# Optimization experiments

Hardware: AMD Instinct MI355X
Metric: run time of the kernel (lower is better)

The kernel has to match this reference:

```python
import jax, jax.numpy as jnp
import numpy as np
from jax import lax

B, C1, C2, CM, H, W, K = 8, 256, 256, 128, 80, 80, 3
N = K * K
PAD = 1
EPS = 1e-5  # nn.BatchNorm2d default eps


def _bn(x, g, b, m, v):
    # eval-mode BatchNorm2d, NCHW
    inv = g / jnp.sqrt(v + EPS)
    return x * inv[None, :, None, None] + (b - m * inv)[None, :, None, None]


def _conv1x1(x, w):  # w: [O, I]
    return jnp.einsum('bihw,oi->bohw', x, w)


def _conv3x3(x, w, b):  # w: [O, I, 3, 3]
    y = lax.conv_general_dilated(x, w, window_strides=(1, 1),
                                 padding=((PAD, PAD), (PAD, PAD)),
                                 dimension_numbers=('NCHW', 'OIHW', 'NCHW'))
    return y + b[None, :, None, None]


def _deform_conv2d(x, offset, mask, w, bias):
    # DCNv2 (torchvision deform_conv2d semantics), stride=1, pad=1, k=3.
    # x: [B,C,H,W]; offset: [B,2N,H,W] pairs (dy,dx) per kernel tap (row-major);
    # mask: [B,N,H,W]; w: [O,C,3,3]
    Bx, C, Hx, Wx = x.shape
    ky, kx = jnp.meshgrid(jnp.arange(K), jnp.arange(K), indexing='ij')
    ky = ky.reshape(N).astype(x.dtype)
    kx = kx.reshape(N).astype(x.dtype)
    off = offset.reshape(Bx, N, 2, Hx, Wx)
    # sampling positions [B,N,H,W]
    py = (jnp.arange(Hx, dtype=x.dtype)[None, None, :, None] - PAD
          + ky[None, :, None, None] + off[:, :, 0])
    px = (jnp.arange(Wx, dtype=x.dtype)[None, None, None, :] - PAD
          + kx[None, :, None, None] + off[:, :, 1])

    y0 = jnp.floor(py)
    x0 = jnp.floor(px)
    wy1 = py - y0  # frac weights
    wx1 = px - x0
    x_flat = x.reshape(Bx, C, Hx * Wx)

    def corner(yi, xi, wgt):
        valid = (yi >= 0) & (yi < Hx) & (xi >= 0) & (xi < Wx)
        yc = jnp.clip(yi, 0, Hx - 1).astype(jnp.int32)
        xc = jnp.clip(xi, 0, Wx - 1).astype(jnp.int32)
        idx = (yc * Wx + xc).reshape(Bx, 1, N * Hx * Wx)
        g = jnp.take_along_axis(x_flat, idx, axis=2).reshape(Bx, C, N, Hx, Wx)
        return g * (wgt * valid.astype(x.dtype))[:, None]

    sampled = (corner(y0, x0, (1 - wy1) * (1 - wx1))
               + corner(y0, x0 + 1, (1 - wy1) * wx1)
               + corner(y0 + 1, x0, wy1 * (1 - wx1))
               + corner(y0 + 1, x0 + 1, wy1 * wx1))
    sampled = sampled * mask[:, None]  # modulated (v2)
    out = jnp.einsum('bcnhw,ocn->bohw', sampled, w.reshape(w.shape[0], C, N))
    return out + bias[None, :, None, None]


def setup_inputs() -> dict:
    key = jax.random.key(0)
    ks = jax.random.split(key, 20)
    f32 = jnp.float32
    d = {}
    d['x'] = jax.random.normal(ks[0], (B, C1, H, W), dtype=f32)
    # cv1: 1x1 conv (no bias) + BN
    d['cv1_w'] = jax.random.normal(ks[1], (CM, C1), dtype=f32) * (1.0 / np.sqrt(C1))
    d['bn1_g'] = jax.random.uniform(ks[2], (CM,), dtype=f32, minval=0.5, maxval=1.5)
    d['bn1_b'] = jax.random.normal(ks[3], (CM,), dtype=f32) * 0.1
    d['bn1_m'] = jax.random.normal(ks[4], (CM,), dtype=f32) * 0.1
    d['bn1_v'] = jax.random.uniform(ks[5], (CM,), dtype=f32, minval=0.5, maxval=1.5)
    # offset conv: predicts 3*N channels (2N offsets + N mask logits)
    d['off_w'] = jax.random.normal(ks[6], (3 * N, CM, K, K), dtype=f32) * 0.01
    d['off_b'] = jax.random.normal(ks[7], (3 * N,), dtype=f32) * 0.1
    # deformable conv main weight/bias
    d['dcn_w'] = jax.random.normal(ks[8], (CM, CM, K, K), dtype=f32) * np.sqrt(2.0 / (CM * N))
    d['dcn_b'] = jnp.zeros((CM,), dtype=f32)
    d['bn2_g'] = jax.random.uniform(ks[9], (CM,), dtype=f32, minval=0.5, maxval=1.5)
    d['bn2_b'] = jax.random.normal(ks[10], (CM,), dtype=f32) * 0.1
    d['bn2_m'] = jax.random.normal(ks[11], (CM,), dtype=f32) * 0.1
    d['bn2_v'] = jax.random.uniform(ks[12], (CM,), dtype=f32, minval=0.5, maxval=1.5)
    # cv3: 1x1 conv + BN
    d['cv3_w'] = jax.random.normal(ks[13], (C2, CM), dtype=f32) * (1.0 / np.sqrt(CM))
    d['bn3_g'] = jax.random.uniform(ks[14], (C2,), dtype=f32, minval=0.5, maxval=1.5)
    d['bn3_b'] = jax.random.normal(ks[15], (C2,), dtype=f32) * 0.1
    d['bn3_m'] = jax.random.normal(ks[16], (C2,), dtype=f32) * 0.1
    d['bn3_v'] = jax.random.uniform(ks[17], (C2,), dtype=f32, minval=0.5, maxval=1.5)
    return d


def reference(x, cv1_w, bn1_g, bn1_b, bn1_m, bn1_v,
              off_w, off_b, dcn_w, dcn_b,
              bn2_g, bn2_b, bn2_m, bn2_v,
              cv3_w, bn3_g, bn3_b, bn3_m, bn3_v):
    y = jax.nn.silu(_bn(_conv1x1(x, cv1_w), bn1_g, bn1_b, bn1_m, bn1_v))
    pred = _conv3x3(y, off_w, off_b)          # [B,3N,H,W]
    offset = pred[:, :2 * N]
    mask = jax.nn.sigmoid(pred[:, 2 * N:])
    y = _deform_conv2d(y, offset, mask, dcn_w, dcn_b)
    y = jax.nn.silu(_bn(y, bn2_g, bn2_b, bn2_m, bn2_v))
    y = jax.nn.silu(_bn(_conv1x1(y, cv3_w), bn3_g, bn3_b, bn3_m, bn3_v))
    return x + y  # shortcut: c1 == c2
```

## Files before the change

kernel.cpp:

```cpp
#include <hip/hip_runtime.h>
#include <math.h>

#define HWX   6400
#define WID   80
#define HGT   80
#define CMID  128
#define CIN   256
#define COUT  256

#define WS_PRED 0
#define WS_BN   1382400
#define WS_Y2   1383424
#define WS_Z2   4660224
#define WS_WPK  7937024
#define WS_WPO  8010752
#define WS_WP1  8029184
#define WS_WP3  8045568

typedef float floatx16 __attribute__((ext_vector_type(16)));
typedef short shortx8  __attribute__((ext_vector_type(8)));
typedef float floatx2  __attribute__((ext_vector_type(2)));

union U8 { uint32_t u[4]; shortx8 s; };

__device__ __forceinline__ float silu_f(float t){ return t / (1.f + __expf(-t)); }
__device__ __forceinline__ float bf16lo(uint32_t u){ return __uint_as_float(u << 16); }
__device__ __forceinline__ float bf16hi(uint32_t u){ return __uint_as_float(u & 0xffff0000u); }
__device__ __forceinline__ uint32_t f2bf(float f){
    uint32_t u = __float_as_uint(f);
    return (u + 0x7fffu + ((u >> 16) & 1u)) >> 16;
}
__device__ __forceinline__ floatx2 up2(uint32_t u){
    floatx2 r; r.x = __uint_as_float(u << 16); r.y = __uint_as_float(u & 0xffff0000u); return r;
}
__device__ __forceinline__ uint32_t pk2(floatx2 v){
    return __builtin_amdgcn_perm(__float_as_uint(v.y) + 0x8000u,
                                 __float_as_uint(v.x) + 0x8000u, 0x07060302u);
}
__device__ __forceinline__ uint32_t pk2f(float a, float b){ floatx2 v; v.x=a; v.y=b; return pk2(v); }

__global__ __launch_bounds__(256) void k0_prep(
    const float* __restrict__ dcn_w, const float* __restrict__ off_w,
    const float* __restrict__ cv1_w, const float* __restrict__ cv3_w,
    const float* __restrict__ g1, const float* __restrict__ b1, const float* __restrict__ m1, const float* __restrict__ v1,
    const float* __restrict__ g2, const float* __restrict__ b2, const float* __restrict__ m2, const float* __restrict__ v2,
    const float* __restrict__ dcn_b,
    const float* __restrict__ g3, const float* __restrict__ b3, const float* __restrict__ m3, const float* __restrict__ v3,
    uint32_t* __restrict__ wpk, uint32_t* __restrict__ wpo,
    uint32_t* __restrict__ wp1, uint32_t* __restrict__ wp3, float* __restrict__ bnw)
{
    int i = blockIdx.x * 256 + threadIdx.x;
    if (i < 4*9*8*256) {
        int j = i & 3, lane = (i >> 2) & 63, s = (i >> 8) & 7;
        int r2 = i >> 11; int tap = r2 % 9, g = r2 / 9;
        int oc = g*32 + (lane & 31);
        int c  = s*16 + ((lane >> 5) << 3) + 2*j;
        wpk[i] = f2bf(dcn_w[(oc*128 + c)*9 + tap]) | (f2bf(dcn_w[(oc*128 + c + 1)*9 + tap]) << 16);
    }
    if (i < 9*8*256) {
        int j = i & 3, lane = (i >> 2) & 63, s = (i >> 8) & 7, tap = i >> 11;
        int oc = lane & 31;
        int c  = s*16 + ((lane >> 5) << 3) + 2*j;
        float lo = (oc < 27) ? off_w[(oc*128 + c)*9 + tap] : 0.f;
        float hi = (oc < 27) ? off_w[(oc*128 + c + 1)*9 + tap] : 0.f;
        wpo[i] = f2bf(lo) | (f2bf(hi) << 16);
    }
    if (i < 4*16*256) {
        int j = i & 3, lane = (i >> 2) & 63, s = (i >> 8) & 15, g = i >> 12;
        int oc = g*32 + (lane & 31);
        int c  = s*16 + ((lane >> 5) << 3) + 2*j;
        wp1[i] = f2bf(cv1_w[oc*256 + c]) | (f2bf(cv1_w[oc*256 + c + 1]) << 16);
    }
    if (i < 8*8*256) {
        int j = i & 3, lane = (i >> 2) & 63, s = (i >> 8) & 7, g = i >> 11;
        int oc = g*32 + (lane & 31);
        int c  = s*16 + ((lane >> 5) << 3) + 2*j;
        wp3[i] = f2bf(cv3_w[oc*128 + c]) | (f2bf(cv3_w[oc*128 + c + 1]) << 16);
    }
    if (i < 128) {
        float inv = g1[i] * rsqrtf(v1[i] + 1e-5f);
        bnw[i] = inv; bnw[128+i] = b1[i] - m1[i]*inv;
    } else if (i < 256) {
        int j = i - 128;
        float inv = g2[j] * rsqrtf(v2[j] + 1e-5f);
        bnw[256+j] = inv; bnw[384+j] = b2[j] - m2[j]*inv + inv*dcn_b[j];
    } else if (i < 512) {
        int j = i - 256;
        float inv = g3[j] * rsqrtf(v3[j] + 1e-5f);
        bnw[512+j] = inv; bnw[768+j] = b3[j] - m3[j]*inv;
    }
}

#define K1PAD 68
__global__ __launch_bounds__(256) void k1_cv1(
    const float* __restrict__ x, const uint32_t* __restrict__ wp1,
    const float* __restrict__ bn, uint32_t* __restrict__ y2)
{
    __shared__ uint32_t L[64*66];
    int blk = blockIdx.x;
    int b = blk / 100, pix0 = (blk % 100) * 64;
    int t = threadIdx.x;
    int lane = t & 63, w = t >> 6;
    int pixl = lane & 31, bhalf = lane >> 5;
    floatx16 acc0 = {}, acc1 = {};
    const float* xb = x + (size_t)b*CIN*HWX + pix0;
    const uint32_t* wpg = wp1 + (size_t)(w*16)*256 + lane*4;

    int r2 = t >> 4, c4 = (t & 15) * 4;
    for (int kk = 0; kk < 256; kk += 32) {
        float4 a0 = *(const float4*)(xb + (size_t)(kk + 2*r2)*HWX + c4);
        float4 a1 = *(const float4*)(xb + (size_t)(kk + 2*r2 + 1)*HWX + c4);
        uint4 q;
        q.x = pk2f(a0.x, a1.x);
        q.y = pk2f(a0.y, a1.y);
        q.z = pk2f(a0.z, a1.z);
        q.w = pk2f(a0.w, a1.w);
        __syncthreads();
        *(uint4*)&L[r2*K1PAD + c4] = q;
        __syncthreads();
        #pragma unroll
        for (int sl = 0; sl < 2; sl++) {
            int s = (kk >> 4) + sl;
            U8 a, b0, b1;
            const uint32_t* as = wpg + s*256;
            a.u[0]=as[0]; a.u[1]=as[1]; a.u[2]=as[2]; a.u[3]=as[3];
            int row = sl*8 + bhalf*4;
            #pragma unroll
            for (int j = 0; j < 4; j++) b0.u[j] = L[(row+j)*K1PAD + pixl];
            #pragma unroll
            for (int j = 0; j < 4; j++) b1.u[j] = L[(row+j)*K1PAD + 32 + pixl];
            acc0 = __builtin_amdgcn_mfma_f32_32x32x16_bf16(a.s, b0.s, acc0, 0, 0, 0);
            acc1 = __builtin_amdgcn_mfma_f32_32x32x16_bf16(a.s, b1.s, acc1, 0, 0, 0);
        }
    }
    __syncthreads();
    #pragma unroll
    for (int r = 0; r < 16; r += 2) {
        int oc = w*32 + (r & 3) + 8*(r >> 2) + 4*bhalf;
        float s0 = bn[oc],   be0 = bn[128+oc];
        float s1 = bn[oc+1], be1 = bn[128+oc+1];
        uint32_t d0 = pk2f(silu_f(acc0[r]*s0+be0), silu_f(acc0[r+1]*s1+be1));
        uint32_t d1 = pk2f(silu_f(acc1[r]*s0+be0), silu_f(acc1[r+1]*s1+be1));
        int oc2 = oc >> 1;
        L[pixl*66 + oc2]        = d0;
        L[(32+pixl)*66 + oc2]   = d1;
    }
    __syncthreads();
    uint32_t* y2b = y2 + (size_t)b*HWX*64 + (size_t)pix0*64;
    int q2 = t & 31, p0 = t >> 5;
    #pragma unroll
    for (int pp = 0; pp < 8; pp++) {
        int pix = p0 + pp*8;
        uint2 v = make_uint2(L[pix*66 + q2*2], L[pix*66 + q2*2 + 1]);
        *(uint2*)(y2b + (size_t)pix*64 + q2*2) = v;
    }
}

__global__ __launch_bounds__(256) void k2_off(
    const uint32_t* __restrict__ y2, const uint32_t* __restrict__ wpo,
    const float* __restrict__ ob, float* __restrict__ pred)
{
    int blk = blockIdx.x;
    int b = blk / 50, pix0 = (blk % 50) * 128;
    int t = threadIdx.x;
    int lane = t & 63, w = t >> 6;
    int pixl = lane & 31, half = lane >> 5;
    int p = pix0 + w*32 + pixl;
    int h = p / WID, xw = p % WID;
    const uint32_t* yb = y2 + (size_t)b*HWX*64;
    floatx16 acc = {};

    for (int tap = 0; tap < 9; tap++) {
        int dy = tap/3 - 1, dx = tap%3 - 1;
        int gh = h + dy, gx = xw + dx;
        bool valid = (gh >= 0) && (gh < HGT) && (gx >= 0) && (gx < WID);
        const uint32_t* pp = yb + (size_t)(gh*WID + gx)*64 + half*4;
        const uint32_t* ap = wpo + (size_t)(tap*8)*256 + lane*4;
        #pragma unroll
        for (int s = 0; s < 8; s++) {
            U8 a, bf;
            const uint32_t* as = ap + s*256;
            a.u[0]=as[0]; a.u[1]=as[1]; a.u[2]=as[2]; a.u[3]=as[3];
            if (valid) {
                uint4 q = *(const uint4*)(pp + s*8);
                bf.u[0]=q.x; bf.u[1]=q.y; bf.u[2]=q.z; bf.u[3]=q.w;
            } else {
                bf.u[0]=0u; bf.u[1]=0u; bf.u[2]=0u; bf.u[3]=0u;
            }
            acc = __builtin_amdgcn_mfma_f32_32x32x16_bf16(a.s, bf.s, acc, 0, 0, 0);
        }
    }
    float* pb = pred + (size_t)b*27*HWX;
    #pragma unroll
    for (int r = 0; r < 16; r++) {
        int oc = (r & 3) + 8*(r >> 2) + 4*half;
        if (oc < 27) {
            float v = acc[r] + ob[oc];
            if (oc >= 18) v = 1.f/(1.f+__expf(-v));
            pb[oc*HWX + p] = v;
        }
    }
}

#define S2S 33
__global__ __launch_bounds__(256) void k3_dcn(
    const uint32_t* __restrict__ y2, const float* __restrict__ pred,
    const uint32_t* __restrict__ wpk, const float* __restrict__ bn, uint32_t* __restrict__ z2)
{
    __shared__ uint32_t S2[64*S2S];
    __shared__ int   sidx[32][4];
    __shared__ float swgt[32][4];
    int blk = blockIdx.x;
    int b = blk / 200, pix0 = (blk % 200) * 32;
    int t = threadIdx.x;
    int lane = t & 63, w = t >> 6;
    int pixl = lane & 31, bhalf = lane >> 5;
    const float* pb = pred + (size_t)b*27*HWX;
    const uint32_t* yb = y2 + (size_t)b*HWX*64;
    floatx16 acc = {};
    int c4 = lane & 31, pixoff = lane >> 5;

    for (int tap = 0; tap < 9; tap++) {
        __syncthreads();
        if (t < 32) {
            int pix = pix0 + t;
            int h = pix / WID, wq = pix % WID;
            float dy = pb[(2*tap)*HWX + pix];
            float dx = pb[(2*tap+1)*HWX + pix];
            float mk = pb[(18+tap)*HWX + pix];
            float pyf = (float)(h - 1 + tap/3) + dy;
            float pxf = (float)(wq - 1 + tap%3) + dx;
            float y0f = floorf(pyf), x0f = floorf(pxf);
            float wy1 = pyf - y0f, wx1 = pxf - x0f;
            int iy0 = (int)y0f, ix0 = (int)x0f;
            int iy1 = iy0 + 1,  ix1 = ix0 + 1;
            float vy0 = (iy0 >= 0 && iy0 < HGT) ? 1.f : 0.f;
            float vy1 = (iy1 >= 0 && iy1 < HGT) ? 1.f : 0.f;
            float vx0 = (ix0 >= 0 && ix0 < WID) ? 1.f : 0.f;
            float vx1 = (ix1 >= 0 && ix1 < WID) ? 1.f : 0.f;
            int cy0 = min(max(iy0,0),HGT-1), cy1 = min(max(iy1,0),HGT-1);
            int cx0 = min(max(ix0,0),WID-1), cx1 = min(max(ix1,0),WID-1);
            sidx[t][0] = cy0*WID+cx0; sidx[t][1] = cy0*WID+cx1;
            sidx[t][2] = cy1*WID+cx0; sidx[t][3] = cy1*WID+cx1;
            swgt[t][0] = (1.f-wy1)*(1.f-wx1)*mk*vy0*vx0;
            swgt[t][1] = (1.f-wy1)*wx1*mk*vy0*vx1;
            swgt[t][2] = wy1*(1.f-wx1)*mk*vy1*vx0;
            swgt[t][3] = wy1*wx1*mk*vy1*vx1;
        }
        __syncthreads();
        #pragma unroll
        for (int p = 0; p < 4; p++) {
            int pix = w*8 + p*2 + pixoff;
            int i0 = sidx[pix][0], i1 = sidx[pix][1], i2 = sidx[pix][2], i3 = sidx[pix][3];
            floatx2 W0, W1, W2, W3;
            W0.x = W0.y = swgt[pix][0]; W1.x = W1.y = swgt[pix][1];
            W2.x = W2.y = swgt[pix][2]; W3.x = W3.y = swgt[pix][3];
            uint2 u0 = *(const uint2*)(yb + (size_t)i0*64 + c4*2);
            uint2 u1 = *(const uint2*)(yb + (size_t)i1*64 + c4*2);
            uint2 u2 = *(const uint2*)(yb + (size_t)i2*64 + c4*2);
            uint2 u3 = *(const uint2*)(yb + (size_t)i3*64 + c4*2);
            floatx2 aX = up2(u0.x) * W0;
            aX = __builtin_elementwise_fma(up2(u1.x), W1, aX);
            aX = __builtin_elementwise_fma(up2(u2.x), W2, aX);
            aX = __builtin_elementwise_fma(up2(u3.x), W3, aX);
            floatx2 aY = up2(u0.y) * W0;
            aY = __builtin_elementwise_fma(up2(u1.y), W1, aY);
            aY = __builtin_elementwise_fma(up2(u2.y), W2, aY);
            aY = __builtin_elementwise_fma(up2(u3.y), W3, aY);
            S2[(c4*2)*S2S + pix]     = pk2(aX);
            S2[(c4*2 + 1)*S2S + pix] = pk2(aY);
        }
        __syncthreads();
        const uint32_t* wp = wpk + (size_t)((w*9 + tap)*8)*256 + lane*4;
        int kb = bhalf * 4;
        #pragma unroll
        for (int s = 0; s < 8; s++) {
            U8 a, bf;
            const uint32_t* wps = wp + s*256;
            a.u[0] = wps[0]; a.u[1] = wps[1]; a.u[2] = wps[2]; a.u[3] = wps[3];
            int c2b = s*8 + kb;
            bf.u[0] = S2[(c2b+0)*S2S + pixl];
            bf.u[1] = S2[(c2b+1)*S2S + pixl];
            bf.u[2] = S2[(c2b+2)*S2S + pixl];
            bf.u[3] = S2[(c2b+3)*S2S + pixl];
            acc = __builtin_amdgcn_mfma_f32_32x32x16_bf16(a.s, bf.s, acc, 0, 0, 0);
        }
    }
    __syncthreads();
    #pragma unroll
    for (int r = 0; r < 16; r += 2) {
        int oc = w*32 + (r & 3) + 8*(r >> 2) + 4*bhalf;
        float s0 = bn[256+oc],   be0 = bn[384+oc];
        float s1 = bn[256+oc+1], be1 = bn[384+oc+1];
        uint32_t d = pk2f(silu_f(acc[r]*s0+be0), silu_f(acc[r+1]*s1+be1));
        S2[pixl*66 + (oc >> 1)] = d;
    }
    __syncthreads();
    uint32_t* z2b = z2 + (size_t)b*HWX*64 + (size_t)pix0*64;
    int q2 = t & 31, p0 = t >> 5;
    #pragma unroll
    for (int pp = 0; pp < 4; pp++) {
        int pix = p0 + pp*8;
        uint2 v = make_uint2(S2[pix*66 + q2*2], S2[pix*66 + q2*2 + 1]);
        *(uint2*)(z2b + (size_t)pix*64 + q2*2) = v;
    }
}

__global__ __launch_bounds__(256) void k4_cv3(
    const uint32_t* __restrict__ z2, const uint32_t* __restrict__ wp3,
    const float* __restrict__ bn, const float* __restrict__ x, float* __restrict__ out)
{
    int blk = blockIdx.x;
    int half = blk & 1, blk2 = blk >> 1;
    int b = blk2 / 100, pix0 = (blk2 % 100) * 64;
    int t = threadIdx.x;
    int lane = t & 63, w = t >> 6;
    int pixl = lane & 31, bhalf = lane >> 5;
    int g = half*4 + w;
    floatx16 acc0 = {}, acc1 = {};
    const uint32_t* zb = z2 + (size_t)b*HWX*64 + (size_t)pix0*64;
    const uint32_t* wpg = wp3 + (size_t)(g*8)*256 + lane*4;

    #pragma unroll
    for (int s = 0; s < 8; s++) {
        U8 a, b0, b1;
        const uint32_t* as = wpg + s*256;
        a.u[0]=as[0]; a.u[1]=as[1]; a.u[2]=as[2]; a.u[3]=as[3];
        uint4 q0 = *(const uint4*)(zb + (size_t)pixl*64 + s*8 + bhalf*4);
        uint4 q1 = *(const uint4*)(zb + (size_t)(32+pixl)*64 + s*8 + bhalf*4);
        b0.u[0]=q0.x; b0.u[1]=q0.y; b0.u[2]=q0.z; b0.u[3]=q0.w;
        b1.u[0]=q1.x; b1.u[1]=q1.y; b1.u[2]=q1.z; b1.u[3]=q1.w;
        acc0 = __builtin_amdgcn_mfma_f32_32x32x16_bf16(a.s, b0.s, acc0, 0, 0, 0);
        acc1 = __builtin_amdgcn_mfma_f32_32x32x16_bf16(a.s, b1.s, acc1, 0, 0, 0);
    }
    const float* xb = x + (size_t)b*COUT*HWX + pix0;
    float* ob = out + (size_t)b*COUT*HWX + pix0;
    #pragma unroll
    for (int r = 0; r < 16; r++) {
        int oc = g*32 + (r & 3) + 8*(r >> 2) + 4*bhalf;
        float sc = bn[512+oc], be = bn[768+oc];
        float v0 = silu_f(acc0[r]*sc+be) + xb[(size_t)oc*HWX + pixl];
        float v1 = silu_f(acc1[r]*sc+be) + xb[(size_t)oc*HWX + 32 + pixl];
        ob[(size_t)oc*HWX + pixl]      = v0;
        ob[(size_t)oc*HWX + 32 + pixl] = v1;
    }
}

extern "C" void kernel_launch(void* const* d_in, const int* in_sizes, int n_in,
                              void* d_out, int out_size, void* d_ws, size_t ws_size,
                              hipStream_t stream) {
    const float* x     = (const float*)d_in[0];
    const float* cv1_w = (const float*)d_in[1];
    const float* bn1_g = (const float*)d_in[2];
    const float* bn1_b = (const float*)d_in[3];
    const float* bn1_m = (const float*)d_in[4];
    const float* bn1_v = (const float*)d_in[5];
    const float* off_w = (const float*)d_in[6];
    const float* off_b = (const float*)d_in[7];
    const float* dcn_w = (const float*)d_in[8];
    const float* dcn_b = (const float*)d_in[9];
    const float* bn2_g = (const float*)d_in[10];
    const float* bn2_b = (const float*)d_in[11];
    const float* bn2_m = (const float*)d_in[12];
    const float* bn2_v = (const float*)d_in[13];
    const float* cv3_w = (const float*)d_in[14];
    const float* bn3_g = (const float*)d_in[15];
    const float* bn3_b = (const float*)d_in[16];
    const float* bn3_m = (const float*)d_in[17];
    const float* bn3_v = (const float*)d_in[18];

    float* ws   = (float*)d_ws;
    float*    PRED = ws + WS_PRED;
    float*    BN   = ws + WS_BN;
    uint32_t* Y2   = (uint32_t*)(ws + WS_Y2);
    uint32_t* Z2   = (uint32_t*)(ws + WS_Z2);
    uint32_t* WPK  = (uint32_t*)(ws + WS_WPK);
    uint32_t* WPO  = (uint32_t*)(ws + WS_WPO);
    uint32_t* WP1  = (uint32_t*)(ws + WS_WP1);
    uint32_t* WP3  = (uint32_t*)(ws + WS_WP3);

    hipLaunchKernelGGL(k0_prep, dim3(288), dim3(256), 0, stream,
        dcn_w, off_w, cv1_w, cv3_w,
        bn1_g, bn1_b, bn1_m, bn1_v,
        bn2_g, bn2_b, bn2_m, bn2_v, dcn_b,
        bn3_g, bn3_b, bn3_m, bn3_v, WPK, WPO, WP1, WP3, BN);
    hipLaunchKernelGGL(k1_cv1, dim3(800), dim3(256), 0, stream, x, WP1, BN, Y2);
    hipLaunchKernelGGL(k2_off, dim3(400), dim3(256), 0, stream, Y2, WPO, off_b, PRED);
    hipLaunchKernelGGL(k3_dcn, dim3(1600), dim3(256), 0, stream, Y2, PRED, WPK, BN, Z2);
    hipLaunchKernelGGL(k4_cv3, dim3(1600), dim3(256), 0, stream, Z2, WP3, BN, x, (float*)d_out);
}
```

Before: 244.2 us.

## Software-pipeline DCN gathers with double-buffered LDS and precomputed tap indices

In the deformable conv kernel, the sampling indices and weights for all 9 taps are now computed once up front by all threads, instead of by 32 threads per tap between two barriers. The bilinear gathers for the next tap are issued before the MFMA loop of the current tap and blended after it, with the staged samples double-buffered in shared memory. This removes one barrier per tap and lets global gather latency overlap with matrix math. The LDS layout also changes to a pixel-major layout with stride 68 so B-operand reads become 128-bit vector loads. The cost is more registers for the in-flight samples and more LDS, which may reduce occupancy.

```diff
diff --git a/kernel.cpp b/kernel.cpp
--- a/kernel.cpp
+++ b/kernel.cpp
@@ -24,8 +24,6 @@
 union U8 { uint32_t u[4]; shortx8 s; };
 
 __device__ __forceinline__ float silu_f(float t){ return t / (1.f + __expf(-t)); }
-__device__ __forceinline__ float bf16lo(uint32_t u){ return __uint_as_float(u << 16); }
-__device__ __forceinline__ float bf16hi(uint32_t u){ return __uint_as_float(u & 0xffff0000u); }
 __device__ __forceinline__ uint32_t f2bf(float f){
     uint32_t u = __float_as_uint(f);
     return (u + 0x7fffu + ((u >> 16) & 1u)) >> 16;
@@ -96,7 +94,7 @@
     const float* __restrict__ x, const uint32_t* __restrict__ wp1,
     const float* __restrict__ bn, uint32_t* __restrict__ y2)
 {
-    __shared__ uint32_t L[64*66];
+    __shared__ __align__(16) uint32_t L[64*66];
     int blk = blockIdx.x;
     int b = blk / 100, pix0 = (blk % 100) * 64;
     int t = threadIdx.x;
@@ -202,14 +200,14 @@
     }
 }
 
-#define S2S 33
+#define S2R 68
 __global__ __launch_bounds__(256) void k3_dcn(
     const uint32_t* __restrict__ y2, const float* __restrict__ pred,
     const uint32_t* __restrict__ wpk, const float* __restrict__ bn, uint32_t* __restrict__ z2)
 {
-    __shared__ uint32_t S2[64*S2S];
-    __shared__ int   sidx[32][4];
-    __shared__ float swgt[32][4];
+    __shared__ __align__(16) uint32_t S2[2][32*S2R];
+    __shared__ __align__(16) int   sidx9[9*32*4];
+    __shared__ __align__(16) float swgt9[9*32*4];
     int blk = blockIdx.x;
     int b = blk / 200, pix0 = (blk % 200) * 32;
     int t = threadIdx.x;
@@ -220,80 +218,123 @@
     floatx16 acc = {};
     int c4 = lane & 31, pixoff = lane >> 5;
 
+    for (int it = t; it < 288; it += 256) {
+        int tap = it >> 5, px = it & 31;
+        int pix = pix0 + px;
+        int h = pix / WID, wq = pix % WID;
+        float dy = pb[(2*tap)*HWX + pix];
+        float dx = pb[(2*tap+1)*HWX + pix];
+        float mk = pb[(18+tap)*HWX + pix];
+        float pyf = (float)(h - 1 + tap/3) + dy;
+        float pxf = (float)(wq - 1 + tap%3) + dx;
+        float y0f = floorf(pyf), x0f = floorf(pxf);
+        float wy1 = pyf - y0f, wx1 = pxf - x0f;
+        int iy0 = (int)y0f, ix0 = (int)x0f;
+        int iy1 = iy0 + 1,  ix1 = ix0 + 1;
+        float vy0 = (iy0 >= 0 && iy0 < HGT) ? 1.f : 0.f;
+        float vy1 = (iy1 >= 0 && iy1 < HGT) ? 1.f : 0.f;
+        float vx0 = (ix0 >= 0 && ix0 < WID) ? 1.f : 0.f;
+        float vx1 = (ix1 >= 0 && ix1 < WID) ? 1.f : 0.f;
+        int cy0 = min(max(iy0,0),HGT-1), cy1 = min(max(iy1,0),HGT-1);
+        int cx0 = min(max(ix0,0),WID-1), cx1 = min(max(ix1,0),WID-1);
+        int base = (tap*32 + px)*4;
+        sidx9[base+0] = cy0*WID+cx0; sidx9[base+1] = cy0*WID+cx1;
+        sidx9[base+2] = cy1*WID+cx0; sidx9[base+3] = cy1*WID+cx1;
+        swgt9[base+0] = (1.f-wy1)*(1.f-wx1)*mk*vy0*vx0;
+        swgt9[base+1] = (1.f-wy1)*wx1*mk*vy0*vx1;
+        swgt9[base+2] = wy1*(1.f-wx1)*mk*vy1*vx0;
+        swgt9[base+3] = wy1*wx1*mk*vy1*vx1;
+    }
+    __syncthreads();
+
+    uint2  u[4][4];
+    float4 W[4];
+    uint2  samp[4];
+
+    #pragma unroll
+    for (int p = 0; p < 4; p++) {
+        int pix = w*8 + p*2 + pixoff;
+        int base = (0*32 + pix)*4;
+        int4 si = *(const int4*)&sidx9[base];
+        W[p] = *(const float4*)&swgt9[base];
+        u[p][0] = *(const uint2*)(yb + (size_t)si.x*64 + c4*2);
+        u[p][1] = *(const uint2*)(yb + (size_t)si.y*64 + c4*2);
+        u[p][2] = *(const uint2*)(yb + (size_t)si.z*64 + c4*2);
+        u[p][3] = *(const uint2*)(yb + (size_t)si.w*64 + c4*2);
+    }
+    #pragma unroll
+    for (int p = 0; p < 4; p++) {
+        floatx2 W0, W1, W2, W3;
+        W0.x = W0.y = W[p].x; W1.x = W1.y = W[p].y;
+        W2.x = W2.y = W[p].z; W3.x = W3.y = W[p].w;
+        floatx2 aX = up2(u[p][0].x) * W0;
+        aX = __builtin_elementwise_fma(up2(u[p][1].x), W1, aX);
+        aX = __builtin_elementwise_fma(up2(u[p][2].x), W2, aX);
+        aX = __builtin_elementwise_fma(up2(u[p][3].x), W3, aX);
+        floatx2 aY = up2(u[p][0].y) * W0;
+        aY = __builtin_elementwise_fma(up2(u[p][1].y), W1, aY);
+        aY = __builtin_elementwise_fma(up2(u[p][2].y), W2, aY);
+        aY = __builtin_elementwise_fma(up2(u[p][3].y), W3, aY);
+        samp[p].x = pk2(aX); samp[p].y = pk2(aY);
+    }
+
+    #pragma unroll
     for (int tap = 0; tap < 9; tap++) {
-        __syncthreads();
-        if (t < 32) {
-            int pix = pix0 + t;
-            int h = pix / WID, wq = pix % WID;
-            float dy = pb[(2*tap)*HWX + pix];
-            float dx = pb[(2*tap+1)*HWX + pix];
-            float mk = pb[(18+tap)*HWX + pix];
-            float pyf = (float)(h - 1 + tap/3) + dy;
-            float pxf = (float)(wq - 1 + tap%3) + dx;
-            float y0f = floorf(pyf), x0f = floorf(pxf);
-            float wy1 = pyf - y0f, wx1 = pxf - x0f;
-            int iy0 = (int)y0f, ix0 = (int)x0f;
-            int iy1 = iy0 + 1,  ix1 = ix0 + 1;
-            float vy0 = (iy0 >= 0 && iy0 < HGT) ? 1.f : 0.f;
-            float vy1 = (iy1 >= 0 && iy1 < HGT) ? 1.f : 0.f;
-            float vx0 = (ix0 >= 0 && ix0 < WID) ? 1.f : 0.f;
-            float vx1 = (ix1 >= 0 && ix1 < WID) ? 1.f : 0.f;
-            int cy0 = min(max(iy0,0),HGT-1), cy1 = min(max(iy1,0),HGT-1);
-            int cx0 = min(max(ix0,0),WID-1), cx1 = min(max(ix1,0),WID-1);
-            sidx[t][0] = cy0*WID+cx0; sidx[t][1] = cy0*WID+cx1;
-            sidx[t][2] = cy1*WID+cx0; sidx[t][3] = cy1*WID+cx1;
-            swgt[t][0] = (1.f-wy1)*(1.f-wx1)*mk*vy0*vx0;
-            swgt[t][1] = (1.f-wy1)*wx1*mk*vy0*vx1;
-            swgt[t][2] = wy1*(1.f-wx1)*mk*vy1*vx0;
-            swgt[t][3] = wy1*wx1*mk*vy1*vx1;
-        }
-        __syncthreads();
+        uint32_t* S = &S2[tap & 1][0];
         #pragma unroll
         for (int p = 0; p < 4; p++) {
             int pix = w*8 + p*2 + pixoff;
-            int i0 = sidx[pix][0], i1 = sidx[pix][1], i2 = sidx[pix][2], i3 = sidx[pix][3];
-            floatx2 W0, W1, W2, W3;
-            W0.x = W0.y = swgt[pix][0]; W1.x = W1.y = swgt[pix][1];
-            W2.x = W2.y = swgt[pix][2]; W3.x = W3.y = swgt[pix][3];
-            uint2 u0 = *(const uint2*)(yb + (size_t)i0*64 + c4*2);
-            uint2 u1 = *(const uint2*)(yb + (size_t)i1*64 + c4*2);
-            uint2 u2 = *(const uint2*)(yb + (size_t)i2*64 + c4*2);
-            uint2 u3 = *(const uint2*)(yb + (size_t)i3*64 + c4*2);
-            floatx2 aX = up2(u0.x) * W0;
-            aX = __builtin_elementwise_fma(up2(u1.x), W1, aX);
-            aX = __builtin_elementwise_fma(up2(u2.x), W2, aX);
-            aX = __builtin_elementwise_fma(up2(u3.x), W3, aX);
-            floatx2 aY = up2(u0.y) * W0;
-            aY = __builtin_elementwise_fma(up2(u1.y), W1, aY);
-            aY = __builtin_elementwise_fma(up2(u2.y), W2, aY);
-            aY = __builtin_elementwise_fma(up2(u3.y), W3, aY);
-            S2[(c4*2)*S2S + pix]     = pk2(aX);
-            S2[(c4*2 + 1)*S2S + pix] = pk2(aY);
+            *(uint2*)&S[pix*S2R + c4*2] = samp[p];
         }
         __syncthreads();
+        if (tap < 8) {
+            #pragma unroll
+            for (int p = 0; p < 4; p++) {
+                int pix = w*8 + p*2 + pixoff;
+                int base = ((tap+1)*32 + pix)*4;
+                int4 si = *(const int4*)&sidx9[base];
+                W[p] = *(const float4*)&swgt9[base];
+                u[p][0] = *(const uint2*)(yb + (size_t)si.x*64 + c4*2);
+                u[p][1] = *(const uint2*)(yb + (size_t)si.y*64 + c4*2);
+                u[p][2] = *(const uint2*)(yb + (size_t)si.z*64 + c4*2);
+                u[p][3] = *(const uint2*)(yb + (size_t)si.w*64 + c4*2);
+            }
+        }
         const uint32_t* wp = wpk + (size_t)((w*9 + tap)*8)*256 + lane*4;
-        int kb = bhalf * 4;
         #pragma unroll
         for (int s = 0; s < 8; s++) {
             U8 a, bf;
             const uint32_t* wps = wp + s*256;
             a.u[0] = wps[0]; a.u[1] = wps[1]; a.u[2] = wps[2]; a.u[3] = wps[3];
-            int c2b = s*8 + kb;
-            bf.u[0] = S2[(c2b+0)*S2S + pixl];
-            bf.u[1] = S2[(c2b+1)*S2S + pixl];
-            bf.u[2] = S2[(c2b+2)*S2S + pixl];
-            bf.u[3] = S2[(c2b+3)*S2S + pixl];
+            uint4 q = *(const uint4*)&S[pixl*S2R + s*8 + bhalf*4];
+            bf.u[0]=q.x; bf.u[1]=q.y; bf.u[2]=q.z; bf.u[3]=q.w;
             acc = __builtin_amdgcn_mfma_f32_32x32x16_bf16(a.s, bf.s, acc, 0, 0, 0);
         }
-    }
-    __syncthreads();
+        if (tap < 8) {
+            #pragma unroll
+            for (int p = 0; p < 4; p++) {
+                floatx2 W0, W1, W2, W3;
+                W0.x = W0.y = W[p].x; W1.x = W1.y = W[p].y;
+                W2.x = W2.y = W[p].z; W3.x = W3.y = W[p].w;
+                floatx2 aX = up2(u[p][0].x) * W0;
+                aX = __builtin_elementwise_fma(up2(u[p][1].x), W1, aX);
+                aX = __builtin_elementwise_fma(up2(u[p][2].x), W2, aX);
+                aX = __builtin_elementwise_fma(up2(u[p][3].x), W3, aX);
+                floatx2 aY = up2(u[p][0].y) * W0;
+                aY = __builtin_elementwise_fma(up2(u[p][1].y), W1, aY);
+                aY = __builtin_elementwise_fma(up2(u[p][2].y), W2, aY);
+                aY = __builtin_elementwise_fma(up2(u[p][3].y), W3, aY);
+                samp[p].x = pk2(aX); samp[p].y = pk2(aY);
+            }
+        }
+    }
+    uint32_t* SE = &S2[1][0];
     #pragma unroll
     for (int r = 0; r < 16; r += 2) {
         int oc = w*32 + (r & 3) + 8*(r >> 2) + 4*bhalf;
         float s0 = bn[256+oc],   be0 = bn[384+oc];
         float s1 = bn[256+oc+1], be1 = bn[384+oc+1];
-        uint32_t d = pk2f(silu_f(acc[r]*s0+be0), silu_f(acc[r+1]*s1+be1));
-        S2[pixl*66 + (oc >> 1)] = d;
+        SE[pixl*S2R + (oc >> 1)] = pk2f(silu_f(acc[r]*s0+be0), silu_f(acc[r+1]*s1+be1));
     }
     __syncthreads();
     uint32_t* z2b = z2 + (size_t)b*HWX*64 + (size_t)pix0*64;
@@ -301,7 +342,7 @@
     #pragma unroll
     for (int pp = 0; pp < 4; pp++) {
         int pix = p0 + pp*8;
-        uint2 v = make_uint2(S2[pix*66 + q2*2], S2[pix*66 + q2*2 + 1]);
+        uint2 v = *(const uint2*)&SE[pix*S2R + q2*2];
         *(uint2*)(z2b + (size_t)pix*64 + q2*2) = v;
     }
 }
```

Result: faster. 238.6 us (-2.3%).
